# Performance work log

Measured on AMD Instinct MI355X. Metric: run time of the kernel, lower is better.

## Reference

```python
import jax, jax.numpy as jnp
import numpy as np

# levels for the auction iterations: j = 7..-1 gives level = -4^j, j = -2 gives level = 0
_LEVEL_JS = list(range(7, -3, -1))


def approx_match(xyz1, xyz2):
    # xyz1: [B,N,3], xyz2: [B,M,3] -> soft match matrix [B,N,M]
    B, N, _ = xyz1.shape
    M = xyz2.shape[1]
    multiL = 1.0 if N >= M else float(M // N)
    multiR = float(N // M) if N >= M else 1.0
    # pairwise squared distances [B,N,M]
    d2 = jnp.sum((xyz1[:, :, None, :] - xyz2[:, None, :, :]) ** 2, axis=-1)
    levels = jnp.array([0.0 if j == -2 else -(4.0 ** j) for j in _LEVEL_JS],
                       dtype=xyz1.dtype)

    def step(carry, level):
        match, remainL, remainR = carry
        w = jnp.exp(level * d2) * remainR[:, None, :]                      # [B,N,M]
        # row-normalize to each left point's remaining mass
        w = w * (remainL / (jnp.sum(w, axis=2) + 1e-9))[:, :, None]
        # clip columns to right points' remaining capacity
        ss = jnp.sum(w, axis=1) + 1e-9                                     # [B,M]
        w = w * jnp.minimum(remainR / ss, 1.0)[:, None, :]
        match = match + w
        remainL = jnp.maximum(remainL - jnp.sum(w, axis=2), 0.0)
        remainR = jnp.maximum(remainR - jnp.sum(w, axis=1), 0.0)
        return (match, remainL, remainR), None

    init = (jnp.zeros_like(d2),
            jnp.full((B, N), multiL, dtype=d2.dtype),
            jnp.full((B, M), multiR, dtype=d2.dtype))
    (match, _, _), _ = jax.lax.scan(step, init, levels)
    return match


def match_cost(xyz1, xyz2, match):
    # cost[b] = sum_{k,l} match[b,k,l] * ||xyz1[b,k] - xyz2[b,l]||
    d = jnp.sqrt(jnp.sum((xyz1[:, :, None, :] - xyz2[:, None, :, :]) ** 2, axis=-1))
    return jnp.sum(match * d, axis=(1, 2))


def setup_inputs() -> dict:
    key = jax.random.key(0)
    k1, k2 = jax.random.split(key)
    B, N, M = 8, 2048, 2048
    input1 = jax.random.normal(k1, (B, N, 3), dtype=jnp.float32)
    input2 = jax.random.normal(k2, (B, M, 3), dtype=jnp.float32)
    return {"input1": input1, "input2": input2}


def reference(input1, input2):
    match = approx_match(input1, input2)
    return match_cost(input1, input2, match)
```

## Files before the change

kernel.cpp:

```cpp
#include <hip/hip_runtime.h>
#include <hip/hip_fp16.h>


#define BATCH 8
#define NPTS 2048
#define MPTS 2048
#define BLOCK 256
#define ROWS 16
#define NSH 8
#define LOG2E 1.44269504088896340736f

__device__ __forceinline__ float fast_exp2(float x) {
  return __builtin_amdgcn_exp2f(x);
}
__device__ __forceinline__ float fast_sqrt(float a) {
  return __builtin_amdgcn_sqrtf(a);
}
__device__ __forceinline__ float packh2(float c, float r) {
  __half2 h = __halves2half2(__float2half_rn(c), __float2half_rn(r));
  return __builtin_bit_cast(float, h);
}

__device__ __forceinline__ void load8(const float4* q, int r0, float k,
                                      float* x, float* y, float* z) {
  int b4 = (r0 >> 2) * 3;
  float4 q0 = q[b4], q1 = q[b4 + 1], q2 = q[b4 + 2];
  float4 q3 = q[b4 + 3], q4 = q[b4 + 4], q5 = q[b4 + 5];
  x[0] = k * q0.x; y[0] = k * q0.y; z[0] = k * q0.z;
  x[1] = k * q0.w; y[1] = k * q1.x; z[1] = k * q1.y;
  x[2] = k * q1.z; y[2] = k * q1.w; z[2] = k * q2.x;
  x[3] = k * q2.y; y[3] = k * q2.z; z[3] = k * q2.w;
  x[4] = k * q3.x; y[4] = k * q3.y; z[4] = k * q3.z;
  x[5] = k * q3.w; y[5] = k * q4.x; z[5] = k * q4.y;
  x[6] = k * q4.z; y[6] = k * q4.w; z[6] = k * q5.x;
  x[7] = k * q5.y; y[7] = k * q5.z; z[7] = k * q5.w;
}

__global__ __launch_bounds__(BLOCK, 4) void emd_A0_kernel(
    const float* __restrict__ xyz1, const float* __restrict__ xyz2,
    float* __restrict__ rowscale, float* __restrict__ out,
    float* __restrict__ t9, float* __restrict__ t1acc,
    float* __restrict__ t1zero, float k0) {
  __shared__ float4 sP[MPTS];
  __shared__ float sRed[ROWS * 4];
  __shared__ float sRs[ROWS];

  const int tid = threadIdx.x;
  const int bid = blockIdx.x;
  const int b = bid >> 7;
  const int blk = bid & 127;
  const int t0 = blk * ROWS;
  if (bid == 0 && tid < BATCH) { out[tid] = 0.0f; t9[tid] = 0.0f; }

  const float4* q2 = (const float4*)(xyz2 + (size_t)b * MPTS * 3);
  float4* z4 = (blk < NSH)
      ? (float4*)(t1zero + ((size_t)blk * BATCH + b) * MPTS) : nullptr;
  for (int g = tid; g < MPTS / 4; g += BLOCK) {
    float4 a = q2[3 * g], bb = q2[3 * g + 1], c = q2[3 * g + 2];
    sP[4 * g + 0] = make_float4(k0 * a.x, k0 * a.y, k0 * a.z, 0.0f);
    sP[4 * g + 1] = make_float4(k0 * a.w, k0 * bb.x, k0 * bb.y, 0.0f);
    sP[4 * g + 2] = make_float4(k0 * bb.z, k0 * bb.w, k0 * c.x, 0.0f);
    sP[4 * g + 3] = make_float4(k0 * c.y, k0 * c.z, k0 * c.w, 0.0f);
    if (z4) z4[g] = make_float4(0.f, 0.f, 0.f, 0.f);
  }
  __syncthreads();

  const int wave = tid >> 6, lane = tid & 63;
  const int phase = lane >> 1, rg = lane & 1;
  const int r0 = t0 + rg * 8;
  float x1[8], y1[8], z1[8], acc[8];
  load8((const float4*)(xyz1 + (size_t)b * NPTS * 3), r0, k0, x1, y1, z1);
#pragma unroll
  for (int j = 0; j < 8; ++j) acc[j] = 0.0f;
  const int mb = wave * 512 + phase;
#pragma unroll 2
  for (int it = 0; it < 16; ++it) {
    float4 v = sP[mb + it * 32];
#pragma unroll
    for (int j = 0; j < 8; ++j) {
      float dx = x1[j] - v.x, dy = y1[j] - v.y, dz = z1[j] - v.z;
      float s = __builtin_fmaf(dx, dx, __builtin_fmaf(dy, dy, dz * dz));
      acc[j] += fast_exp2(-s);
    }
  }
#pragma unroll
  for (int j = 0; j < 8; ++j) {
    acc[j] += __shfl_xor(acc[j], 2, 64);
    acc[j] += __shfl_xor(acc[j], 4, 64);
    acc[j] += __shfl_xor(acc[j], 8, 64);
    acc[j] += __shfl_xor(acc[j], 16, 64);
    acc[j] += __shfl_xor(acc[j], 32, 64);
  }
  if (lane < 2) {
#pragma unroll
    for (int j = 0; j < 8; ++j) sRed[(rg * 8 + j) * 4 + wave] = acc[j];
  }
  __syncthreads();
  if (tid < ROWS) {
    float s = sRed[tid * 4] + sRed[tid * 4 + 1] + sRed[tid * 4 + 2] +
              sRed[tid * 4 + 3];
    float rs = 1.0f / (s + 1e-9f);
    rowscale[(size_t)b * NPTS + t0 + tid] = rs;
    sRs[tid] = rs;
  }
  __syncthreads();

  float rsn[8];
#pragma unroll
  for (int j = 0; j < 8; ++j) rsn[j] = sRs[rg * 8 + j];
  float* accb = t1acc + ((size_t)(blk & (NSH - 1)) * BATCH + b) * MPTS;
#pragma unroll 2
  for (int it = 0; it < 16; ++it) {
    int idx = mb + it * 32;
    float4 v = sP[idx];
    float part = 0.0f;
#pragma unroll
    for (int j = 0; j < 8; ++j) {
      float dx = x1[j] - v.x, dy = y1[j] - v.y, dz = z1[j] - v.z;
      float s = __builtin_fmaf(dx, dx, __builtin_fmaf(dy, dy, dz * dz));
      part = __builtin_fmaf(fast_exp2(-s), rsn[j], part);
    }
    part += __shfl_xor(part, 1, 64);
    if (rg == 0) atomicAdd(accb + idx, part);
  }
}

template <bool FIRST, bool LAST>
__global__ __launch_bounds__(BLOCK, 4) void emd_CA_kernel(
    const float* __restrict__ xyz1, const float* __restrict__ xyz2,
    float* __restrict__ rowscale, float* __restrict__ remainL,
    const float* __restrict__ rrIn, float* __restrict__ rrOut,
    const float* __restrict__ t1In, float* __restrict__ t1Acc,
    float* __restrict__ t1Zero, float* __restrict__ out,
    float* __restrict__ t9, float kS, float invK) {
  __shared__ float4 sP[MPTS];
  __shared__ float sRedS[ROWS * 4];
  __shared__ float sRedC[ROWS * 4];
  __shared__ float sRedR[ROWS * 4];
  __shared__ float sCost[ROWS];
  __shared__ float sRs[ROWS];

  const int tid = threadIdx.x;
  const int bid = blockIdx.x;
  const int b = bid >> 7;
  const int blk = bid & 127;
  const int t0 = blk * ROWS;
  const bool desig = blk == 0;

  const float4* q2 = (const float4*)(xyz2 + (size_t)b * MPTS * 3);
  const float4* rr4 = (const float4*)(rrIn + (size_t)b * MPTS);
  const float4* t14 = (const float4*)(t1In + (size_t)b * MPTS);
  const size_t sh4 = (size_t)BATCH * MPTS / 4;
  float4* ro4 = (float4*)(rrOut + (size_t)b * MPTS);
  float4* z4 = (!LAST && blk < NSH)
      ? (float4*)(t1Zero + ((size_t)blk * BATCH + b) * MPTS) : nullptr;
  for (int g = tid; g < MPTS / 4; g += BLOCK) {
    float4 a = q2[3 * g], bb = q2[3 * g + 1], c = q2[3 * g + 2];
    float4 t1v = t14[g];
#pragma unroll
    for (int cpy = 1; cpy < NSH; ++cpy) {
      float4 tv = t14[cpy * sh4 + g];
      t1v.x += tv.x; t1v.y += tv.y; t1v.z += tv.z; t1v.w += tv.w;
    }
    float4 rrv = FIRST ? make_float4(1.f, 1.f, 1.f, 1.f) : rr4[g];
    float cc[4], rn[4];
    float rrc[4] = {rrv.x, rrv.y, rrv.z, rrv.w};
    float t1c[4] = {t1v.x, t1v.y, t1v.z, t1v.w};
#pragma unroll
    for (int i = 0; i < 4; ++i) {
      float colsum = rrc[i] * t1c[i];
      float cs = fminf(rrc[i] / (colsum + 1e-9f), 1.0f);
      cc[i] = rrc[i] * cs;
      rn[i] = fmaxf(rrc[i] - colsum * cs, 0.0f);
    }
    sP[4 * g + 0] = make_float4(kS * a.x, kS * a.y, kS * a.z, packh2(cc[0], rn[0]));
    sP[4 * g + 1] = make_float4(kS * a.w, kS * bb.x, kS * bb.y, packh2(cc[1], rn[1]));
    sP[4 * g + 2] = make_float4(kS * bb.z, kS * bb.w, kS * c.x, packh2(cc[2], rn[2]));
    sP[4 * g + 3] = make_float4(kS * c.y, kS * c.z, kS * c.w, packh2(cc[3], rn[3]));
    if (desig) ro4[g] = make_float4(rn[0], rn[1], rn[2], rn[3]);
    if (z4) z4[g] = make_float4(0.f, 0.f, 0.f, 0.f);
  }
  __syncthreads();

  const int wave = tid >> 6, lane = tid & 63;
  const int phase = lane >> 2, rg = lane & 3;
  const int r0 = t0 + rg * 4;
  float x1[4], y1[4], z1[4];
  {
    const float4* q1 = (const float4*)(xyz1 + (size_t)b * NPTS * 3);
    int b4 = (r0 >> 2) * 3;
    float4 a = q1[b4], bb = q1[b4 + 1], c = q1[b4 + 2];
    x1[0] = kS * a.x;  y1[0] = kS * a.y;  z1[0] = kS * a.z;
    x1[1] = kS * a.w;  y1[1] = kS * bb.x; z1[1] = kS * bb.y;
    x1[2] = kS * bb.z; y1[2] = kS * bb.w; z1[2] = kS * c.x;
    x1[3] = kS * c.y;  y1[3] = kS * c.z;  z1[3] = kS * c.w;
  }
  float accS[4] = {0.f, 0.f, 0.f, 0.f};
  float accC[4] = {0.f, 0.f, 0.f, 0.f};
  float accR[4] = {0.f, 0.f, 0.f, 0.f};
  const int mb = wave * 512 + phase;
#pragma unroll 4
  for (int it = 0; it < 32; ++it) {
    float4 v = sP[mb + it * 16];
    __half2 h = __builtin_bit_cast(__half2, v.w);
    float cc = __low2float(h);
    float rr = __high2float(h);
#pragma unroll
    for (int j = 0; j < 4; ++j) {
      float dx = x1[j] - v.x, dy = y1[j] - v.y, dz = z1[j] - v.z;
      float s = __builtin_fmaf(dx, dx, __builtin_fmaf(dy, dy, dz * dz));
      float sq = fast_sqrt(s);
      float e1, e2;
      if (LAST) {
        e2 = 1.0f;
        e1 = fast_exp2(-s);
      } else {
        e2 = fast_exp2(-s);
        float e2s = e2 * e2;
        e1 = e2s * e2s;
      }
      float t = e1 * cc;
      accS[j] += t;
      accC[j] = __builtin_fmaf(t, sq, accC[j]);
      if (LAST) accR[j] += rr;
      else      accR[j] = __builtin_fmaf(e2, rr, accR[j]);
    }
  }
#pragma unroll
  for (int j = 0; j < 4; ++j) {
    accS[j] += __shfl_xor(accS[j], 4, 64);
    accS[j] += __shfl_xor(accS[j], 8, 64);
    accS[j] += __shfl_xor(accS[j], 16, 64);
    accS[j] += __shfl_xor(accS[j], 32, 64);
    accC[j] += __shfl_xor(accC[j], 4, 64);
    accC[j] += __shfl_xor(accC[j], 8, 64);
    accC[j] += __shfl_xor(accC[j], 16, 64);
    accC[j] += __shfl_xor(accC[j], 32, 64);
    accR[j] += __shfl_xor(accR[j], 4, 64);
    accR[j] += __shfl_xor(accR[j], 8, 64);
    accR[j] += __shfl_xor(accR[j], 16, 64);
    accR[j] += __shfl_xor(accR[j], 32, 64);
  }
  if (lane < 4) {
#pragma unroll
    for (int j = 0; j < 4; ++j) {
      sRedS[(rg * 4 + j) * 4 + wave] = accS[j];
      sRedC[(rg * 4 + j) * 4 + wave] = accC[j];
      sRedR[(rg * 4 + j) * 4 + wave] = accR[j];
    }
  }
  __syncthreads();
  if (tid < ROWS) {
    float S2 = sRedS[tid * 4] + sRedS[tid * 4 + 1] + sRedS[tid * 4 + 2] +
               sRedS[tid * 4 + 3];
    float C = sRedC[tid * 4] + sRedC[tid * 4 + 1] + sRedC[tid * 4 + 2] +
              sRedC[tid * 4 + 3];
    float R = sRedR[tid * 4] + sRedR[tid * 4 + 1] + sRedR[tid * 4 + 2] +
              sRedR[tid * 4 + 3];
    size_t idx = (size_t)b * NPTS + t0 + tid;
    float rs = rowscale[idx];
    float rl = FIRST ? 1.0f : remainL[idx];
    float rlN = fmaxf(rl - rs * S2, 0.0f);
    remainL[idx] = rlN;
    float rsN = rlN / (R + 1e-9f);
    rowscale[idx] = rsN;
    sCost[tid] = rs * C * invK;
    sRs[tid] = rsN;
  }
  __syncthreads();
  if (tid == 0) {
    float t = 0.0f;
#pragma unroll
    for (int i = 0; i < ROWS; ++i) t += sCost[i];
    atomicAdd(out + b, t);
    if (LAST) {
      float r = 0.0f;
#pragma unroll
      for (int i = 0; i < ROWS; ++i) r += sRs[i];
      atomicAdd(t9 + b, r);
    }
  }
  if (!LAST) {
    float rsn[4];
#pragma unroll
    for (int j = 0; j < 4; ++j) rsn[j] = sRs[rg * 4 + j];
    float* accb = t1Acc + ((size_t)(blk & (NSH - 1)) * BATCH + b) * MPTS;
#pragma unroll 4
    for (int it = 0; it < 32; ++it) {
      int idx = mb + it * 16;
      float4 v = sP[idx];
      float part = 0.0f;
#pragma unroll
      for (int j = 0; j < 4; ++j) {
        float dx = x1[j] - v.x, dy = y1[j] - v.y, dz = z1[j] - v.z;
        float s = __builtin_fmaf(dx, dx, __builtin_fmaf(dy, dy, dz * dz));
        part = __builtin_fmaf(fast_exp2(-s), rsn[j], part);
      }
      part += __shfl_xor(part, 1, 64);
      part += __shfl_xor(part, 2, 64);
      if (rg == 0) atomicAdd(accb + idx, part);
    }
  }
}

__global__ __launch_bounds__(BLOCK, 4) void emd_C9_kernel(
    const float* __restrict__ xyz1, const float* __restrict__ xyz2,
    const float* __restrict__ rowscale, const float* __restrict__ remainR,
    const float* __restrict__ t9, float* __restrict__ out) {
  __shared__ float4 sP[MPTS];
  __shared__ float sRed[ROWS * 4];
  __shared__ float sCost[ROWS];

  const int tid = threadIdx.x;
  const int bid = blockIdx.x;
  const int b = bid >> 7;
  const int t0 = (bid & 127) * ROWS;
  const int wave = tid >> 6, lane = tid & 63;
  const float t1 = t9[b];

  const float4* q2 = (const float4*)(xyz2 + (size_t)b * MPTS * 3);
  const float4* rr4 = (const float4*)(remainR + (size_t)b * MPTS);
  for (int g = tid; g < MPTS / 4; g += BLOCK) {
    float4 a = q2[3 * g], bb = q2[3 * g + 1], c = q2[3 * g + 2];
    float4 rr = rr4[g];
    float w0 = rr.x * fminf(rr.x / (rr.x * t1 + 1e-9f), 1.0f);
    float w1 = rr.y * fminf(rr.y / (rr.y * t1 + 1e-9f), 1.0f);
    float w2 = rr.z * fminf(rr.z / (rr.z * t1 + 1e-9f), 1.0f);
    float w3 = rr.w * fminf(rr.w / (rr.w * t1 + 1e-9f), 1.0f);
    sP[4 * g + 0] = make_float4(a.x, a.y, a.z, w0);
    sP[4 * g + 1] = make_float4(a.w, bb.x, bb.y, w1);
    sP[4 * g + 2] = make_float4(bb.z, bb.w, c.x, w2);
    sP[4 * g + 3] = make_float4(c.y, c.z, c.w, w3);
  }
  __syncthreads();

  const int phase = lane >> 1, rg = lane & 1;
  const int r0 = t0 + rg * 8;
  float x1[8], y1[8], z1[8], acc[8];
  load8((const float4*)(xyz1 + (size_t)b * NPTS * 3), r0, 1.0f, x1, y1, z1);
#pragma unroll
  for (int j = 0; j < 8; ++j) acc[j] = 0.0f;
  const int mb = wave * 512 + phase;
#pragma unroll 2
  for (int it = 0; it < 16; ++it) {
    float4 v = sP[mb + it * 32];
#pragma unroll
    for (int j = 0; j < 8; ++j) {
      float dx = x1[j] - v.x, dy = y1[j] - v.y, dz = z1[j] - v.z;
      float d2 = __builtin_fmaf(dx, dx, __builtin_fmaf(dy, dy, dz * dz));
      acc[j] = __builtin_fmaf(fast_sqrt(d2), v.w, acc[j]);
    }
  }
#pragma unroll
  for (int j = 0; j < 8; ++j) {
    acc[j] += __shfl_xor(acc[j], 2, 64);
    acc[j] += __shfl_xor(acc[j], 4, 64);
    acc[j] += __shfl_xor(acc[j], 8, 64);
    acc[j] += __shfl_xor(acc[j], 16, 64);
    acc[j] += __shfl_xor(acc[j], 32, 64);
  }
  if (lane < 2) {
#pragma unroll
    for (int j = 0; j < 8; ++j) sRed[(rg * 8 + j) * 4 + wave] = acc[j];
  }
  __syncthreads();
  if (tid < ROWS) {
    float C = sRed[tid * 4] + sRed[tid * 4 + 1] + sRed[tid * 4 + 2] +
              sRed[tid * 4 + 3];
    sCost[tid] = rowscale[(size_t)b * NPTS + t0 + tid] * C;
  }
  __syncthreads();
  if (tid == 0) {
    float t = 0.0f;
#pragma unroll
    for (int i = 0; i < ROWS; ++i) t += sCost[i];
    atomicAdd(out + b, t);
  }
}

extern "C" void kernel_launch(void* const* d_in, const int* in_sizes, int n_in,
                              void* d_out, int out_size, void* d_ws, size_t ws_size,
                              hipStream_t stream) {
  const float* xyz1 = (const float*)d_in[0];
  const float* xyz2 = (const float*)d_in[1];
  float* out = (float*)d_out;
  float* ws = (float*)d_ws;

  const int BN = BATCH * NPTS, BM = BATCH * MPTS;
  const size_t TBUF = (size_t)NSH * BM;
  float* remainL  = ws;
  float* rowscale = ws + BN;
  float* rrA      = ws + 2 * BN;
  float* rrB      = ws + 2 * BN + BM;
  float* t1b      = ws + 2 * BN + 2 * BM;
  float* t9       = ws + 2 * BN + 2 * BM + 3 * TBUF;

  const float levels[9] = {-16384.f, -4096.f, -1024.f, -256.f, -64.f,
                           -16.f,    -4.f,    -1.f,    -0.25f};
  dim3 grid(BATCH * (NPTS / ROWS));

  hipMemsetAsync(t1b, 0, TBUF * sizeof(float), stream);

  emd_A0_kernel<<<grid, BLOCK, 0, stream>>>(
      xyz1, xyz2, rowscale, out, t9, t1b , t1b + TBUF ,
      sqrtf(-levels[0] * LOG2E));

  for (int l = 0; l < 9; ++l) {
    float kB = sqrtf(-levels[l] * LOG2E);
    float kA = 0.5f * kB;
    float* cur = t1b + (size_t)(l % 3) * TBUF;
    float* nxt = t1b + (size_t)((l + 1) % 3) * TBUF;
    float* zer = t1b + (size_t)((l + 2) % 3) * TBUF;
    float* rin = (l % 2 == 0) ? rrA : rrB;
    float* rou = (l % 2 == 0) ? rrB : rrA;
    if (l == 0) {
      emd_CA_kernel<true, false><<<grid, BLOCK, 0, stream>>>(
          xyz1, xyz2, rowscale, remainL, rin, rou, cur, nxt, zer, out, t9,
          kA, 1.0f / kA);
    } else if (l < 8) {
      emd_CA_kernel<false, false><<<grid, BLOCK, 0, stream>>>(
          xyz1, xyz2, rowscale, remainL, rin, rou, cur, nxt, zer, out, t9,
          kA, 1.0f / kA);
    } else {
      emd_CA_kernel<false, true><<<grid, BLOCK, 0, stream>>>(
          xyz1, xyz2, rowscale, remainL, rin, rou, cur, nxt, zer, out, t9,
          kB, 1.0f / kB);
    }
  }
  emd_C9_kernel<<<grid, BLOCK, 0, stream>>>(xyz1, xyz2, rowscale, rrB, t9, out);
}
```

Baseline: 357.9 us.

## Stream right-point tiles through half-size LDS chunks to double occupancy

```diff
diff --git a/kernel.cpp b/kernel.cpp
--- a/kernel.cpp
+++ b/kernel.cpp
@@ -7,6 +7,7 @@
 #define MPTS 2048
 #define BLOCK 256
 #define ROWS 16
+#define CHUNK 1024
 #define NSH 8
 #define LOG2E 1.44269504088896340736f
 
@@ -36,12 +37,12 @@
   x[7] = k * q5.y; y[7] = k * q5.z; z[7] = k * q5.w;
 }
 
-__global__ __launch_bounds__(BLOCK, 4) void emd_A0_kernel(
+__global__ __launch_bounds__(BLOCK, 8) void emd_A0_kernel(
     const float* __restrict__ xyz1, const float* __restrict__ xyz2,
     float* __restrict__ rowscale, float* __restrict__ out,
     float* __restrict__ t9, float* __restrict__ t1acc,
     float* __restrict__ t1zero, float k0) {
-  __shared__ float4 sP[MPTS];
+  __shared__ float4 sP[CHUNK];
   __shared__ float sRed[ROWS * 4];
   __shared__ float sRs[ROWS];
 
@@ -52,35 +53,41 @@
   const int t0 = blk * ROWS;
   if (bid == 0 && tid < BATCH) { out[tid] = 0.0f; t9[tid] = 0.0f; }
 
+  const int wave = tid >> 6, lane = tid & 63;
+  const int phase = lane >> 1, rg = lane & 1;
+  const int r0 = t0 + rg * 8;
   const float4* q2 = (const float4*)(xyz2 + (size_t)b * MPTS * 3);
   float4* z4 = (blk < NSH)
       ? (float4*)(t1zero + ((size_t)blk * BATCH + b) * MPTS) : nullptr;
-  for (int g = tid; g < MPTS / 4; g += BLOCK) {
-    float4 a = q2[3 * g], bb = q2[3 * g + 1], c = q2[3 * g + 2];
-    sP[4 * g + 0] = make_float4(k0 * a.x, k0 * a.y, k0 * a.z, 0.0f);
-    sP[4 * g + 1] = make_float4(k0 * a.w, k0 * bb.x, k0 * bb.y, 0.0f);
-    sP[4 * g + 2] = make_float4(k0 * bb.z, k0 * bb.w, k0 * c.x, 0.0f);
-    sP[4 * g + 3] = make_float4(k0 * c.y, k0 * c.z, k0 * c.w, 0.0f);
-    if (z4) z4[g] = make_float4(0.f, 0.f, 0.f, 0.f);
-  }
-  __syncthreads();
-
-  const int wave = tid >> 6, lane = tid & 63;
-  const int phase = lane >> 1, rg = lane & 1;
-  const int r0 = t0 + rg * 8;
+
   float x1[8], y1[8], z1[8], acc[8];
   load8((const float4*)(xyz1 + (size_t)b * NPTS * 3), r0, k0, x1, y1, z1);
 #pragma unroll
   for (int j = 0; j < 8; ++j) acc[j] = 0.0f;
-  const int mb = wave * 512 + phase;
+  const int mb = wave * 256 + phase;
+
+  for (int ch = 0; ch < 2; ++ch) {
+    __syncthreads();
+    {
+      const float4* qc = q2 + ch * 768;
+      int g = tid;
+      float4 a = qc[3 * g], bb = qc[3 * g + 1], c = qc[3 * g + 2];
+      sP[4 * g + 0] = make_float4(k0 * a.x, k0 * a.y, k0 * a.z, 0.0f);
+      sP[4 * g + 1] = make_float4(k0 * a.w, k0 * bb.x, k0 * bb.y, 0.0f);
+      sP[4 * g + 2] = make_float4(k0 * bb.z, k0 * bb.w, k0 * c.x, 0.0f);
+      sP[4 * g + 3] = make_float4(k0 * c.y, k0 * c.z, k0 * c.w, 0.0f);
+      if (z4) z4[ch * 256 + g] = make_float4(0.f, 0.f, 0.f, 0.f);
+    }
+    __syncthreads();
 #pragma unroll 2
-  for (int it = 0; it < 16; ++it) {
-    float4 v = sP[mb + it * 32];
-#pragma unroll
-    for (int j = 0; j < 8; ++j) {
-      float dx = x1[j] - v.x, dy = y1[j] - v.y, dz = z1[j] - v.z;
-      float s = __builtin_fmaf(dx, dx, __builtin_fmaf(dy, dy, dz * dz));
-      acc[j] += fast_exp2(-s);
+    for (int it = 0; it < 8; ++it) {
+      float4 v = sP[mb + it * 32];
+#pragma unroll
+      for (int j = 0; j < 8; ++j) {
+        float dx = x1[j] - v.x, dy = y1[j] - v.y, dz = z1[j] - v.z;
+        float s = __builtin_fmaf(dx, dx, __builtin_fmaf(dy, dy, dz * dz));
+        acc[j] += fast_exp2(-s);
+      }
     }
   }
 #pragma unroll
@@ -109,31 +116,44 @@
 #pragma unroll
   for (int j = 0; j < 8; ++j) rsn[j] = sRs[rg * 8 + j];
   float* accb = t1acc + ((size_t)(blk & (NSH - 1)) * BATCH + b) * MPTS;
+  for (int ch = 0; ch < 2; ++ch) {
+    __syncthreads();
+    {
+      const float4* qc = q2 + ch * 768;
+      int g = tid;
+      float4 a = qc[3 * g], bb = qc[3 * g + 1], c = qc[3 * g + 2];
+      sP[4 * g + 0] = make_float4(k0 * a.x, k0 * a.y, k0 * a.z, 0.0f);
+      sP[4 * g + 1] = make_float4(k0 * a.w, k0 * bb.x, k0 * bb.y, 0.0f);
+      sP[4 * g + 2] = make_float4(k0 * bb.z, k0 * bb.w, k0 * c.x, 0.0f);
+      sP[4 * g + 3] = make_float4(k0 * c.y, k0 * c.z, k0 * c.w, 0.0f);
+    }
+    __syncthreads();
 #pragma unroll 2
-  for (int it = 0; it < 16; ++it) {
-    int idx = mb + it * 32;
-    float4 v = sP[idx];
-    float part = 0.0f;
-#pragma unroll
-    for (int j = 0; j < 8; ++j) {
-      float dx = x1[j] - v.x, dy = y1[j] - v.y, dz = z1[j] - v.z;
-      float s = __builtin_fmaf(dx, dx, __builtin_fmaf(dy, dy, dz * dz));
-      part = __builtin_fmaf(fast_exp2(-s), rsn[j], part);
-    }
-    part += __shfl_xor(part, 1, 64);
-    if (rg == 0) atomicAdd(accb + idx, part);
+    for (int it = 0; it < 8; ++it) {
+      int idx = mb + it * 32;
+      float4 v = sP[idx];
+      float part = 0.0f;
+#pragma unroll
+      for (int j = 0; j < 8; ++j) {
+        float dx = x1[j] - v.x, dy = y1[j] - v.y, dz = z1[j] - v.z;
+        float s = __builtin_fmaf(dx, dx, __builtin_fmaf(dy, dy, dz * dz));
+        part = __builtin_fmaf(fast_exp2(-s), rsn[j], part);
+      }
+      part += __shfl_xor(part, 1, 64);
+      if (rg == 0) atomicAdd(accb + ch * CHUNK + idx, part);
+    }
   }
 }
 
 template <bool FIRST, bool LAST>
-__global__ __launch_bounds__(BLOCK, 4) void emd_CA_kernel(
+__global__ __launch_bounds__(BLOCK, 8) void emd_CA_kernel(
     const float* __restrict__ xyz1, const float* __restrict__ xyz2,
     float* __restrict__ rowscale, float* __restrict__ remainL,
     const float* __restrict__ rrIn, float* __restrict__ rrOut,
     const float* __restrict__ t1In, float* __restrict__ t1Acc,
     float* __restrict__ t1Zero, float* __restrict__ out,
     float* __restrict__ t9, float kS, float invK) {
-  __shared__ float4 sP[MPTS];
+  __shared__ float4 sP[CHUNK];
   __shared__ float sRedS[ROWS * 4];
   __shared__ float sRedC[ROWS * 4];
   __shared__ float sRedR[ROWS * 4];
@@ -146,6 +166,9 @@
   const int blk = bid & 127;
   const int t0 = blk * ROWS;
   const bool desig = blk == 0;
+  const int wave = tid >> 6, lane = tid & 63;
+  const int phase = lane >> 2, rg = lane & 3;
+  const int r0 = t0 + rg * 4;
 
   const float4* q2 = (const float4*)(xyz2 + (size_t)b * MPTS * 3);
   const float4* rr4 = (const float4*)(rrIn + (size_t)b * MPTS);
@@ -154,37 +177,7 @@
   float4* ro4 = (float4*)(rrOut + (size_t)b * MPTS);
   float4* z4 = (!LAST && blk < NSH)
       ? (float4*)(t1Zero + ((size_t)blk * BATCH + b) * MPTS) : nullptr;
-  for (int g = tid; g < MPTS / 4; g += BLOCK) {
-    float4 a = q2[3 * g], bb = q2[3 * g + 1], c = q2[3 * g + 2];
-    float4 t1v = t14[g];
-#pragma unroll
-    for (int cpy = 1; cpy < NSH; ++cpy) {
-      float4 tv = t14[cpy * sh4 + g];
-      t1v.x += tv.x; t1v.y += tv.y; t1v.z += tv.z; t1v.w += tv.w;
-    }
-    float4 rrv = FIRST ? make_float4(1.f, 1.f, 1.f, 1.f) : rr4[g];
-    float cc[4], rn[4];
-    float rrc[4] = {rrv.x, rrv.y, rrv.z, rrv.w};
-    float t1c[4] = {t1v.x, t1v.y, t1v.z, t1v.w};
-#pragma unroll
-    for (int i = 0; i < 4; ++i) {
-      float colsum = rrc[i] * t1c[i];
-      float cs = fminf(rrc[i] / (colsum + 1e-9f), 1.0f);
-      cc[i] = rrc[i] * cs;
-      rn[i] = fmaxf(rrc[i] - colsum * cs, 0.0f);
-    }
-    sP[4 * g + 0] = make_float4(kS * a.x, kS * a.y, kS * a.z, packh2(cc[0], rn[0]));
-    sP[4 * g + 1] = make_float4(kS * a.w, kS * bb.x, kS * bb.y, packh2(cc[1], rn[1]));
-    sP[4 * g + 2] = make_float4(kS * bb.z, kS * bb.w, kS * c.x, packh2(cc[2], rn[2]));
-    sP[4 * g + 3] = make_float4(kS * c.y, kS * c.z, kS * c.w, packh2(cc[3], rn[3]));
-    if (desig) ro4[g] = make_float4(rn[0], rn[1], rn[2], rn[3]);
-    if (z4) z4[g] = make_float4(0.f, 0.f, 0.f, 0.f);
-  }
-  __syncthreads();
-
-  const int wave = tid >> 6, lane = tid & 63;
-  const int phase = lane >> 2, rg = lane & 3;
-  const int r0 = t0 + rg * 4;
+
   float x1[4], y1[4], z1[4];
   {
     const float4* q1 = (const float4*)(xyz1 + (size_t)b * NPTS * 3);
@@ -198,32 +191,65 @@
   float accS[4] = {0.f, 0.f, 0.f, 0.f};
   float accC[4] = {0.f, 0.f, 0.f, 0.f};
   float accR[4] = {0.f, 0.f, 0.f, 0.f};
-  const int mb = wave * 512 + phase;
+  const int mb = wave * 256 + phase;
+
+  for (int ch = 0; ch < 2; ++ch) {
+    __syncthreads();
+    {
+      const float4* qc = q2 + ch * 768;
+      int g = tid;
+      float4 a = qc[3 * g], bb = qc[3 * g + 1], c = qc[3 * g + 2];
+      float4 t1v = t14[ch * 256 + g];
+#pragma unroll
+      for (int cpy = 1; cpy < NSH; ++cpy) {
+        float4 tv = t14[cpy * sh4 + ch * 256 + g];
+        t1v.x += tv.x; t1v.y += tv.y; t1v.z += tv.z; t1v.w += tv.w;
+      }
+      float4 rrv = FIRST ? make_float4(1.f, 1.f, 1.f, 1.f) : rr4[ch * 256 + g];
+      float cc[4], rn[4];
+      float rrc[4] = {rrv.x, rrv.y, rrv.z, rrv.w};
+      float t1c[4] = {t1v.x, t1v.y, t1v.z, t1v.w};
+#pragma unroll
+      for (int i = 0; i < 4; ++i) {
+        float colsum = rrc[i] * t1c[i];
+        float cs = fminf(rrc[i] / (colsum + 1e-9f), 1.0f);
+        cc[i] = rrc[i] * cs;
+        rn[i] = fmaxf(rrc[i] - colsum * cs, 0.0f);
+      }
+      sP[4 * g + 0] = make_float4(kS * a.x, kS * a.y, kS * a.z, packh2(cc[0], rn[0]));
+      sP[4 * g + 1] = make_float4(kS * a.w, kS * bb.x, kS * bb.y, packh2(cc[1], rn[1]));
+      sP[4 * g + 2] = make_float4(kS * bb.z, kS * bb.w, kS * c.x, packh2(cc[2], rn[2]));
+      sP[4 * g + 3] = make_float4(kS * c.y, kS * c.z, kS * c.w, packh2(cc[3], rn[3]));
+      if (desig) ro4[ch * 256 + g] = make_float4(rn[0], rn[1], rn[2], rn[3]);
+      if (z4) z4[ch * 256 + g] = make_float4(0.f, 0.f, 0.f, 0.f);
+    }
+    __syncthreads();
 #pragma unroll 4
-  for (int it = 0; it < 32; ++it) {
-    float4 v = sP[mb + it * 16];
-    __half2 h = __builtin_bit_cast(__half2, v.w);
-    float cc = __low2float(h);
-    float rr = __high2float(h);
-#pragma unroll
-    for (int j = 0; j < 4; ++j) {
-      float dx = x1[j] - v.x, dy = y1[j] - v.y, dz = z1[j] - v.z;
-      float s = __builtin_fmaf(dx, dx, __builtin_fmaf(dy, dy, dz * dz));
-      float sq = fast_sqrt(s);
-      float e1, e2;
-      if (LAST) {
-        e2 = 1.0f;
-        e1 = fast_exp2(-s);
-      } else {
-        e2 = fast_exp2(-s);
-        float e2s = e2 * e2;
-        e1 = e2s * e2s;
-      }
-      float t = e1 * cc;
-      accS[j] += t;
-      accC[j] = __builtin_fmaf(t, sq, accC[j]);
-      if (LAST) accR[j] += rr;
-      else      accR[j] = __builtin_fmaf(e2, rr, accR[j]);
+    for (int it = 0; it < 16; ++it) {
+      float4 v = sP[mb + it * 16];
+      __half2 h = __builtin_bit_cast(__half2, v.w);
+      float cc = __low2float(h);
+      float rr = __high2float(h);
+#pragma unroll
+      for (int j = 0; j < 4; ++j) {
+        float dx = x1[j] - v.x, dy = y1[j] - v.y, dz = z1[j] - v.z;
+        float s = __builtin_fmaf(dx, dx, __builtin_fmaf(dy, dy, dz * dz));
+        float sq = fast_sqrt(s);
+        float e1, e2;
+        if (LAST) {
+          e2 = 1.0f;
+          e1 = fast_exp2(-s);
+        } else {
+          e2 = fast_exp2(-s);
+          float e2s = e2 * e2;
+          e1 = e2s * e2s;
+        }
+        float t = e1 * cc;
+        accS[j] += t;
+        accC[j] = __builtin_fmaf(t, sq, accC[j]);
+        if (LAST) accR[j] += rr;
+        else      accR[j] = __builtin_fmaf(e2, rr, accR[j]);
+      }
     }
   }
 #pragma unroll
@@ -285,29 +311,42 @@
 #pragma unroll
     for (int j = 0; j < 4; ++j) rsn[j] = sRs[rg * 4 + j];
     float* accb = t1Acc + ((size_t)(blk & (NSH - 1)) * BATCH + b) * MPTS;
+    for (int ch = 0; ch < 2; ++ch) {
+      __syncthreads();
+      {
+        const float4* qc = q2 + ch * 768;
+        int g = tid;
+        float4 a = qc[3 * g], bb = qc[3 * g + 1], c = qc[3 * g + 2];
+        sP[4 * g + 0] = make_float4(kS * a.x, kS * a.y, kS * a.z, 0.0f);
+        sP[4 * g + 1] = make_float4(kS * a.w, kS * bb.x, kS * bb.y, 0.0f);
+        sP[4 * g + 2] = make_float4(kS * bb.z, kS * bb.w, kS * c.x, 0.0f);
+        sP[4 * g + 3] = make_float4(kS * c.y, kS * c.z, kS * c.w, 0.0f);
+      }
+      __syncthreads();
 #pragma unroll 4
-    for (int it = 0; it < 32; ++it) {
-      int idx = mb + it * 16;
-      float4 v = sP[idx];
-      float part = 0.0f;
-#pragma unroll
-      for (int j = 0; j < 4; ++j) {
-        float dx = x1[j] - v.x, dy = y1[j] - v.y, dz = z1[j] - v.z;
-        float s = __builtin_fmaf(dx, dx, __builtin_fmaf(dy, dy, dz * dz));
-        part = __builtin_fmaf(fast_exp2(-s), rsn[j], part);
-      }
-      part += __shfl_xor(part, 1, 64);
-      part += __shfl_xor(part, 2, 64);
-      if (rg == 0) atomicAdd(accb + idx, part);
-    }
-  }
-}
-
-__global__ __launch_bounds__(BLOCK, 4) void emd_C9_kernel(
+      for (int it = 0; it < 16; ++it) {
+        int idx = mb + it * 16;
+        float4 v = sP[idx];
+        float part = 0.0f;
+#pragma unroll
+        for (int j = 0; j < 4; ++j) {
+          float dx = x1[j] - v.x, dy = y1[j] - v.y, dz = z1[j] - v.z;
+          float s = __builtin_fmaf(dx, dx, __builtin_fmaf(dy, dy, dz * dz));
+          part = __builtin_fmaf(fast_exp2(-s), rsn[j], part);
+        }
+        part += __shfl_xor(part, 1, 64);
+        part += __shfl_xor(part, 2, 64);
+        if (rg == 0) atomicAdd(accb + ch * CHUNK + idx, part);
+      }
+    }
+  }
+}
+
+__global__ __launch_bounds__(BLOCK, 8) void emd_C9_kernel(
     const float* __restrict__ xyz1, const float* __restrict__ xyz2,
     const float* __restrict__ rowscale, const float* __restrict__ remainR,
     const float* __restrict__ t9, float* __restrict__ out) {
-  __shared__ float4 sP[MPTS];
+  __shared__ float4 sP[CHUNK];
   __shared__ float sRed[ROWS * 4];
   __shared__ float sCost[ROWS];
 
@@ -316,39 +355,45 @@
   const int b = bid >> 7;
   const int t0 = (bid & 127) * ROWS;
   const int wave = tid >> 6, lane = tid & 63;
+  const int phase = lane >> 1, rg = lane & 1;
+  const int r0 = t0 + rg * 8;
   const float t1 = t9[b];
 
   const float4* q2 = (const float4*)(xyz2 + (size_t)b * MPTS * 3);
   const float4* rr4 = (const float4*)(remainR + (size_t)b * MPTS);
-  for (int g = tid; g < MPTS / 4; g += BLOCK) {
-    float4 a = q2[3 * g], bb = q2[3 * g + 1], c = q2[3 * g + 2];
-    float4 rr = rr4[g];
-    float w0 = rr.x * fminf(rr.x / (rr.x * t1 + 1e-9f), 1.0f);
-    float w1 = rr.y * fminf(rr.y / (rr.y * t1 + 1e-9f), 1.0f);
-    float w2 = rr.z * fminf(rr.z / (rr.z * t1 + 1e-9f), 1.0f);
-    float w3 = rr.w * fminf(rr.w / (rr.w * t1 + 1e-9f), 1.0f);
-    sP[4 * g + 0] = make_float4(a.x, a.y, a.z, w0);
-    sP[4 * g + 1] = make_float4(a.w, bb.x, bb.y, w1);
-    sP[4 * g + 2] = make_float4(bb.z, bb.w, c.x, w2);
-    sP[4 * g + 3] = make_float4(c.y, c.z, c.w, w3);
-  }
-  __syncthreads();
-
-  const int phase = lane >> 1, rg = lane & 1;
-  const int r0 = t0 + rg * 8;
+
   float x1[8], y1[8], z1[8], acc[8];
   load8((const float4*)(xyz1 + (size_t)b * NPTS * 3), r0, 1.0f, x1, y1, z1);
 #pragma unroll
   for (int j = 0; j < 8; ++j) acc[j] = 0.0f;
-  const int mb = wave * 512 + phase;
+  const int mb = wave * 256 + phase;
+
+  for (int ch = 0; ch < 2; ++ch) {
+    __syncthreads();
+    {
+      const float4* qc = q2 + ch * 768;
+      int g = tid;
+      float4 a = qc[3 * g], bb = qc[3 * g + 1], c = qc[3 * g + 2];
+      float4 rr = rr4[ch * 256 + g];
+      float w0 = rr.x * fminf(rr.x / (rr.x * t1 + 1e-9f), 1.0f);
+      float w1 = rr.y * fminf(rr.y / (rr.y * t1 + 1e-9f), 1.0f);
+      float w2 = rr.z * fminf(rr.z / (rr.z * t1 + 1e-9f), 1.0f);
+      float w3 = rr.w * fminf(rr.w / (rr.w * t1 + 1e-9f), 1.0f);
+      sP[4 * g + 0] = make_float4(a.x, a.y, a.z, w0);
+      sP[4 * g + 1] = make_float4(a.w, bb.x, bb.y, w1);
+      sP[4 * g + 2] = make_float4(bb.z, bb.w, c.x, w2);
+      sP[4 * g + 3] = make_float4(c.y, c.z, c.w, w3);
+    }
+    __syncthreads();
 #pragma unroll 2
-  for (int it = 0; it < 16; ++it) {
-    float4 v = sP[mb + it * 32];
-#pragma unroll
-    for (int j = 0; j < 8; ++j) {
-      float dx = x1[j] - v.x, dy = y1[j] - v.y, dz = z1[j] - v.z;
-      float d2 = __builtin_fmaf(dx, dx, __builtin_fmaf(dy, dy, dz * dz));
-      acc[j] = __builtin_fmaf(fast_sqrt(d2), v.w, acc[j]);
+    for (int it = 0; it < 8; ++it) {
+      float4 v = sP[mb + it * 32];
+#pragma unroll
+      for (int j = 0; j < 8; ++j) {
+        float dx = x1[j] - v.x, dy = y1[j] - v.y, dz = z1[j] - v.z;
+        float d2 = __builtin_fmaf(dx, dx, __builtin_fmaf(dy, dy, dz * dz));
+        acc[j] = __builtin_fmaf(fast_sqrt(d2), v.w, acc[j]);
+      }
     }
   }
 #pragma unroll
@@ -402,7 +447,7 @@
   hipMemsetAsync(t1b, 0, TBUF * sizeof(float), stream);
 
   emd_A0_kernel<<<grid, BLOCK, 0, stream>>>(
-      xyz1, xyz2, rowscale, out, t9, t1b , t1b + TBUF ,
+      xyz1, xyz2, rowscale, out, t9, t1b, t1b + TBUF,
       sqrtf(-levels[0] * LOG2E));
 
   for (int l = 0; l < 9; ++l) {
```

Measured after the change: 409.2 us. +14.3%, slower.
